# Kernel tuning notes

Measured on AMD Instinct MI355X. Metric: run time of the kernel, lower is better.

The kernel has to match this reference:

```python
import jax, jax.numpy as jnp
import numpy as np

N, E, F_IN, H, C = 10000, 640000, 128, 128, 40


def setup_inputs() -> dict:
    key = jax.random.key(0)
    ks = jax.random.split(key, 8)
    x = jax.random.normal(ks[0], (N, F_IN), dtype=jnp.float32)
    edge_index = jax.random.randint(ks[1], (2, E), 0, N, dtype=jnp.int64)
    W1 = jax.random.normal(ks[2], (F_IN, H), dtype=jnp.float32) / np.sqrt(F_IN)
    b1 = jnp.zeros((H,), dtype=jnp.float32)
    W2 = jax.random.normal(ks[3], (H, H), dtype=jnp.float32) / np.sqrt(H)
    b2 = jnp.zeros((H,), dtype=jnp.float32)
    Wc = jax.random.normal(ks[4], (H, C), dtype=jnp.float32) / np.sqrt(H)
    bc = jnp.zeros((C,), dtype=jnp.float32)
    return {"x": x, "edge_index": edge_index, "W1": W1, "b1": b1,
            "W2": W2, "b2": b2, "Wc": Wc, "bc": bc}


def _gcn_conv(x, src, dst, norm, W, b):
    # GCNConv: out = D^{-1/2}(A+I)D^{-1/2} (x @ W) + b
    h = x @ W                               # [N, H]
    msg = h[src] * norm[:, None]            # gather + per-edge normalize
    out = jax.ops.segment_sum(msg, dst, num_segments=N)  # scatter-add
    return out + b


def reference(x, edge_index, W1, b1, W2, b2, Wc, bc):
    # add self-loops (as PyG GCNConv does by default)
    loops = jnp.arange(N, dtype=edge_index.dtype)
    src = jnp.concatenate([edge_index[0], loops])   # [E+N]
    dst = jnp.concatenate([edge_index[1], loops])   # [E+N]
    # symmetric normalization deg^{-1/2} with self-loops included
    deg = jax.ops.segment_sum(jnp.ones_like(dst, dtype=x.dtype), dst, num_segments=N)
    dinv = jax.lax.rsqrt(deg)                       # deg >= 1 due to self-loops
    norm = dinv[src] * dinv[dst]                    # [E+N]

    h = _gcn_conv(x, src, dst, norm, W1, b1)
    h = jax.nn.relu(h)
    h = _gcn_conv(h, src, dst, norm, W2, b2)
    logits = h @ Wc + bc                            # [N, C]
    return jax.nn.log_softmax(logits, axis=1)
```

## Files before the change

kernel.cpp:

```cpp
#include <hip/hip_runtime.h>
#include <hip/hip_fp16.h>
#include <math.h>

#define FDIM 128
#define CDIM 40
#define DMAX 192
#define NMAX 10240
#define SLICE_SHIFT 14
#define SLICE_SZ (1 << SLICE_SHIFT)

__device__ __forceinline__ uint2 pack_half4(float4 v) {
    __half2 p0 = __float22half2_rn(make_float2(v.x, v.y));
    __half2 p1 = __float22half2_rn(make_float2(v.z, v.w));
    uint2 u;
    u.x = *(unsigned int*)&p0;
    u.y = *(unsigned int*)&p1;
    return u;
}

__device__ __forceinline__ void upadd(float& a0, float& a1, unsigned int u) {
    __half2 h = *(__half2*)&u;
    float2 f = __half22float2(h);
    a0 += f.x; a1 += f.y;
}

__global__ __launch_bounds__(1024) void k_hist(
        const int* __restrict__ dst, unsigned short* __restrict__ lrank,
        int* __restrict__ cnt, int e, int n) {
    __shared__ int h[NMAX];
    int tid = threadIdx.x;
    for (int i = tid; i < n; i += 1024) h[i] = 0;
    __syncthreads();
    int base = (int)blockIdx.x << SLICE_SHIFT;
    int end = base + SLICE_SZ; if (end > e) end = e;
    for (int i = base + tid * 4; i < end; i += 4096) {
        if (i + 3 < end) {
            int4 d = *(const int4*)(dst + i);
            int p0 = atomicAdd(&h[d.x], 1);
            int p1 = atomicAdd(&h[d.y], 1);
            int p2 = atomicAdd(&h[d.z], 1);
            int p3 = atomicAdd(&h[d.w], 1);
            ushort4 r;
            r.x = (unsigned short)p0; r.y = (unsigned short)p1;
            r.z = (unsigned short)p2; r.w = (unsigned short)p3;
            *(ushort4*)(lrank + i) = r;
        } else {
            for (int k = i; k < end; ++k)
                lrank[k] = (unsigned short)atomicAdd(&h[dst[k]], 1);
        }
    }
    __syncthreads();
    int* c = cnt + (size_t)blockIdx.x * n;
    for (int i = tid; i < n; i += 1024) c[i] = h[i];
}

__global__ __launch_bounds__(256) void k_scan(
        int* __restrict__ cnt, int* __restrict__ deg, int nslice, int n) {
    int v = blockIdx.x * 256 + threadIdx.x;
    if (v >= n) return;
    int s = 0;
    for (int b = 0; b < nslice; ++b) {
        int t = cnt[(size_t)b * n + v];
        cnt[(size_t)b * n + v] = s;
        s += t;
    }
    deg[v] = s;
}

__global__ __launch_bounds__(256) void k_mega(
        const float* __restrict__ A, const float* __restrict__ W,
        const int* __restrict__ deg, uint2* __restrict__ h16, int n,
        const int* __restrict__ src, const int* __restrict__ dst,
        const unsigned short* __restrict__ lrank, const int* __restrict__ base,
        unsigned short* __restrict__ col, int e, int gemm_blocks) {
    __shared__ float As[32][FDIM];
    int tid = threadIdx.x;
    if ((int)blockIdx.x < gemm_blocks) {
        int r0 = blockIdx.x * 32;
        for (int t = tid; t < 32 * 32; t += 256) {
            int r = t >> 5, c4 = t & 31;
            int gr = r0 + r;
            float4 v = make_float4(0.f, 0.f, 0.f, 0.f);
            if (gr < n) v = ((const float4*)A)[(size_t)gr * 32 + c4];
            ((float4*)As[r])[c4] = v;
        }
        __syncthreads();
        int cb = (tid & 31) * 4;
        int rb = (tid >> 5) * 4;
        float4 acc0 = make_float4(0,0,0,0), acc1 = acc0, acc2 = acc0, acc3 = acc0;
        for (int k = 0; k < FDIM; ++k) {
            float4 w = *(const float4*)(W + k * FDIM + cb);
            float a0 = As[rb + 0][k], a1 = As[rb + 1][k];
            float a2 = As[rb + 2][k], a3 = As[rb + 3][k];
            acc0.x += a0 * w.x; acc0.y += a0 * w.y; acc0.z += a0 * w.z; acc0.w += a0 * w.w;
            acc1.x += a1 * w.x; acc1.y += a1 * w.y; acc1.z += a1 * w.z; acc1.w += a1 * w.w;
            acc2.x += a2 * w.x; acc2.y += a2 * w.y; acc2.z += a2 * w.z; acc2.w += a2 * w.w;
            acc3.x += a3 * w.x; acc3.y += a3 * w.y; acc3.z += a3 * w.z; acc3.w += a3 * w.w;
        }
        float4 accs[4] = {acc0, acc1, acc2, acc3};
        #pragma unroll
        for (int i = 0; i < 4; ++i) {
            int gr = r0 + rb + i;
            if (gr < n) {
                float dinv = rsqrtf((float)(deg[gr] + 1));
                float4 v = accs[i];
                v.x *= dinv; v.y *= dinv; v.z *= dinv; v.w *= dinv;
                h16[(size_t)gr * 32 + (cb >> 2)] = pack_half4(v);
            }
        }
    } else {
        int g = ((int)blockIdx.x - gemm_blocks) * 256 + tid;
        int i4 = g * 4;
        if (i4 + 3 < e) {
            const int* bs = base + (size_t)(i4 >> SLICE_SHIFT) * n;
            int4 d = ((const int4*)dst)[g];
            int4 s = ((const int4*)src)[g];
            ushort4 lr = ((const ushort4*)lrank)[g];
            int p0 = bs[d.x] + lr.x;
            int p1 = bs[d.y] + lr.y;
            int p2 = bs[d.z] + lr.z;
            int p3 = bs[d.w] + lr.w;
            if (p0 < DMAX) col[(size_t)d.x * DMAX + p0] = (unsigned short)s.x;
            if (p1 < DMAX) col[(size_t)d.y * DMAX + p1] = (unsigned short)s.y;
            if (p2 < DMAX) col[(size_t)d.z * DMAX + p2] = (unsigned short)s.z;
            if (p3 < DMAX) col[(size_t)d.w * DMAX + p3] = (unsigned short)s.w;
        } else if (i4 < e) {
            for (int k = i4; k < e; ++k) {
                int d = dst[k];
                int p = base[(size_t)(k >> SLICE_SHIFT) * n + d] + lrank[k];
                if (p < DMAX) col[(size_t)d * DMAX + p] = (unsigned short)src[k];
            }
        }
    }
}

__device__ __forceinline__ void wave_gather(
        float& o0, float& o1, const unsigned int* __restrict__ hs,
        const unsigned short* __restrict__ col, int node, int dn, int lane) {
    float a0 = 0.f, a1 = 0.f, b0 = 0.f, b1 = 0.f;
    upadd(a0, a1, hs[(size_t)node * 64 + lane]);
    const uint4* cl8 = (const uint4*)(col + (size_t)node * DMAX);
    int j = 0;
    for (; j + 16 <= dn; j += 16) {
        uint4 cA = cl8[(j >> 3)];
        uint4 cB = cl8[(j >> 3) + 1];
        int s0 = cA.x & 0xFFFF, s1 = cA.x >> 16;
        int s2 = cA.y & 0xFFFF, s3 = cA.y >> 16;
        int s4 = cA.z & 0xFFFF, s5 = cA.z >> 16;
        int s6 = cA.w & 0xFFFF, s7 = cA.w >> 16;
        int s8 = cB.x & 0xFFFF, s9 = cB.x >> 16;
        int sa = cB.y & 0xFFFF, sb = cB.y >> 16;
        int sc = cB.z & 0xFFFF, sd = cB.z >> 16;
        int se = cB.w & 0xFFFF, sf = cB.w >> 16;
        unsigned int q0 = hs[(size_t)s0 * 64 + lane];
        unsigned int q1 = hs[(size_t)s1 * 64 + lane];
        unsigned int q2 = hs[(size_t)s2 * 64 + lane];
        unsigned int q3 = hs[(size_t)s3 * 64 + lane];
        unsigned int q4 = hs[(size_t)s4 * 64 + lane];
        unsigned int q5 = hs[(size_t)s5 * 64 + lane];
        unsigned int q6 = hs[(size_t)s6 * 64 + lane];
        unsigned int q7 = hs[(size_t)s7 * 64 + lane];
        unsigned int q8 = hs[(size_t)s8 * 64 + lane];
        unsigned int q9 = hs[(size_t)s9 * 64 + lane];
        unsigned int qa = hs[(size_t)sa * 64 + lane];
        unsigned int qb = hs[(size_t)sb * 64 + lane];
        unsigned int qc = hs[(size_t)sc * 64 + lane];
        unsigned int qd = hs[(size_t)sd * 64 + lane];
        unsigned int qe = hs[(size_t)se * 64 + lane];
        unsigned int qf = hs[(size_t)sf * 64 + lane];
        upadd(a0, a1, q0); upadd(b0, b1, q1);
        upadd(a0, a1, q2); upadd(b0, b1, q3);
        upadd(a0, a1, q4); upadd(b0, b1, q5);
        upadd(a0, a1, q6); upadd(b0, b1, q7);
        upadd(a0, a1, q8); upadd(b0, b1, q9);
        upadd(a0, a1, qa); upadd(b0, b1, qb);
        upadd(a0, a1, qc); upadd(b0, b1, qd);
        upadd(a0, a1, qe); upadd(b0, b1, qf);
    }
    for (; j + 8 <= dn; j += 8) {
        uint4 c = cl8[j >> 3];
        int s0 = c.x & 0xFFFF, s1 = c.x >> 16;
        int s2 = c.y & 0xFFFF, s3 = c.y >> 16;
        int s4 = c.z & 0xFFFF, s5 = c.z >> 16;
        int s6 = c.w & 0xFFFF, s7 = c.w >> 16;
        unsigned int q0 = hs[(size_t)s0 * 64 + lane];
        unsigned int q1 = hs[(size_t)s1 * 64 + lane];
        unsigned int q2 = hs[(size_t)s2 * 64 + lane];
        unsigned int q3 = hs[(size_t)s3 * 64 + lane];
        unsigned int q4 = hs[(size_t)s4 * 64 + lane];
        unsigned int q5 = hs[(size_t)s5 * 64 + lane];
        unsigned int q6 = hs[(size_t)s6 * 64 + lane];
        unsigned int q7 = hs[(size_t)s7 * 64 + lane];
        upadd(a0, a1, q0); upadd(b0, b1, q1);
        upadd(a0, a1, q2); upadd(b0, b1, q3);
        upadd(a0, a1, q4); upadd(b0, b1, q5);
        upadd(a0, a1, q6); upadd(b0, b1, q7);
    }
    const unsigned short* cl = col + (size_t)node * DMAX;
    for (; j < dn; ++j) upadd(a0, a1, hs[(size_t)cl[j] * 64 + lane]);
    o0 = a0 + b0;
    o1 = a1 + b1;
}

__global__ __launch_bounds__(512) void k_agg1(
        const unsigned int* __restrict__ hs1, const unsigned short* __restrict__ col,
        const int* __restrict__ deg, const float* __restrict__ b1,
        float* __restrict__ a1, int n) {
    int node = (blockIdx.x * 512 + threadIdx.x) >> 6;
    int lane = threadIdx.x & 63;
    if (node >= n) return;
    int dn = deg[node];
    float dinv = rsqrtf((float)(dn + 1));
    if (dn > DMAX) dn = DMAX;
    float o0, o1;
    wave_gather(o0, o1, hs1, col, node, dn, lane);
    float2 bb = ((const float2*)b1)[lane];
    float v0 = fmaxf(dinv * o0 + bb.x, 0.f);
    float v1 = fmaxf(dinv * o1 + bb.y, 0.f);
    ((float2*)a1)[(size_t)node * 64 + lane] = make_float2(v0, v1);
}

__global__ __launch_bounds__(256) void k_gemm2(
        const float* __restrict__ A, const float* __restrict__ W,
        const int* __restrict__ deg, uint2* __restrict__ h16, int n) {
    __shared__ float As[32][FDIM];
    int tid = threadIdx.x;
    int r0 = blockIdx.x * 32;
    for (int t = tid; t < 32 * 32; t += 256) {
        int r = t >> 5, c4 = t & 31;
        int gr = r0 + r;
        float4 v = make_float4(0.f, 0.f, 0.f, 0.f);
        if (gr < n) v = ((const float4*)A)[(size_t)gr * 32 + c4];
        ((float4*)As[r])[c4] = v;
    }
    __syncthreads();
    int cb = (tid & 31) * 4;
    int rb = (tid >> 5) * 4;
    float4 acc0 = make_float4(0,0,0,0), acc1 = acc0, acc2 = acc0, acc3 = acc0;
    for (int k = 0; k < FDIM; ++k) {
        float4 w = *(const float4*)(W + k * FDIM + cb);
        float a0 = As[rb + 0][k], a1 = As[rb + 1][k];
        float a2 = As[rb + 2][k], a3 = As[rb + 3][k];
        acc0.x += a0 * w.x; acc0.y += a0 * w.y; acc0.z += a0 * w.z; acc0.w += a0 * w.w;
        acc1.x += a1 * w.x; acc1.y += a1 * w.y; acc1.z += a1 * w.z; acc1.w += a1 * w.w;
        acc2.x += a2 * w.x; acc2.y += a2 * w.y; acc2.z += a2 * w.z; acc2.w += a2 * w.w;
        acc3.x += a3 * w.x; acc3.y += a3 * w.y; acc3.z += a3 * w.z; acc3.w += a3 * w.w;
    }
    float4 accs[4] = {acc0, acc1, acc2, acc3};
    #pragma unroll
    for (int i = 0; i < 4; ++i) {
        int gr = r0 + rb + i;
        if (gr < n) {
            float dinv = rsqrtf((float)(deg[gr] + 1));
            float4 v = accs[i];
            v.x *= dinv; v.y *= dinv; v.z *= dinv; v.w *= dinv;
            h16[(size_t)gr * 32 + (cb >> 2)] = pack_half4(v);
        }
    }
}

__global__ __launch_bounds__(512) void k_agg2c(
        const unsigned int* __restrict__ hs2, const unsigned short* __restrict__ col,
        const int* __restrict__ deg, const float* __restrict__ b2,
        const float* __restrict__ Wc, const float* __restrict__ bc,
        float* __restrict__ out, int n) {
    __shared__ float As[8][FDIM];
    int tid = threadIdx.x;
    int wv = tid >> 6, lane = tid & 63;
    int node = blockIdx.x * 8 + wv;
    if (node < n) {
        int dn = deg[node];
        float dinv = rsqrtf((float)(dn + 1));
        if (dn > DMAX) dn = DMAX;
        float o0, o1;
        wave_gather(o0, o1, hs2, col, node, dn, lane);
        float2 bb = ((const float2*)b2)[lane];
        ((float2*)As[wv])[lane] = make_float2(dinv * o0 + bb.x, dinv * o1 + bb.y);
    }
    __syncthreads();
    if (node >= n) return;
    const float* row = As[wv];
    int c = (lane < CDIM) ? lane : (lane - 24);
    float acc = bc[c];
    for (int k = 0; k < FDIM; k += 4) {
        float a0 = row[k + 0], a1 = row[k + 1];
        float a2 = row[k + 2], a3 = row[k + 3];
        acc += a0 * Wc[(k + 0) * CDIM + c];
        acc += a1 * Wc[(k + 1) * CDIM + c];
        acc += a2 * Wc[(k + 2) * CDIM + c];
        acc += a3 * Wc[(k + 3) * CDIM + c];
    }
    float lv = (lane < CDIM) ? acc : -INFINITY;
    float m = lv;
    for (int off = 32; off > 0; off >>= 1) m = fmaxf(m, __shfl_down(m, off));
    m = __shfl(m, 0);
    float e = (lane < CDIM) ? expf(lv - m) : 0.0f;
    float s = e;
    for (int off = 32; off > 0; off >>= 1) s += __shfl_down(s, off);
    s = __shfl(s, 0);
    if (lane < CDIM) out[(size_t)node * CDIM + lane] = lv - m - logf(s);
}


extern "C" void kernel_launch(void* const* d_in, const int* in_sizes, int n_in,
                              void* d_out, int out_size, void* d_ws, size_t ws_size,
                              hipStream_t stream) {
    const float* x  = (const float*)d_in[0];
    const int*   ei = (const int*)d_in[1];
    const float* W1 = (const float*)d_in[2];
    const float* b1 = (const float*)d_in[3];
    const float* W2 = (const float*)d_in[4];
    const float* b2 = (const float*)d_in[5];
    const float* Wc = (const float*)d_in[6];
    const float* bc = (const float*)d_in[7];
    float* out = (float*)d_out;

    const int N = in_sizes[0] / FDIM;
    const int E = in_sizes[1] / 2;
    const int* srcp = ei;
    const int* dstp = ei + E;
    const int NSLICE = (E + SLICE_SZ - 1) >> SLICE_SHIFT;

    char* ws = (char*)d_ws;
    auto alloc = [&](size_t bytes) {
        char* p = ws;
        ws += (bytes + 255) & ~(size_t)255;
        return p;
    };
    int*            deg   = (int*)           alloc((size_t)N * 4);
    int*            cnt   = (int*)           alloc((size_t)NSLICE * N * 4);
    unsigned short* lrank = (unsigned short*)alloc((size_t)E * 2);
    unsigned short* col   = (unsigned short*)alloc((size_t)N * DMAX * 2);
    uint4*          h1h   = (uint4*)         alloc((size_t)N * 256);
    uint4*          h2h   = (uint4*)         alloc((size_t)N * 256);
    float*          a1    = (float*)         alloc((size_t)N * FDIM * 4);

    k_hist<<<NSLICE, 1024, 0, stream>>>(dstp, lrank, cnt, E, N);

    k_scan<<<(N + 255) / 256, 256, 0, stream>>>(cnt, deg, NSLICE, N);

    int gb = (N + 31) / 32;
    int fb = (E / 4 + 255) / 256;
    k_mega<<<gb + fb, 256, 0, stream>>>(
        x, W1, deg, (uint2*)h1h, N, srcp, dstp, lrank, cnt, col, E, gb);

    k_agg1<<<((size_t)N * 64 + 511) / 512, 512, 0, stream>>>(
        (const unsigned int*)h1h, col, deg, b1, a1, N);

    k_gemm2<<<(N + 31) / 32, 256, 0, stream>>>(
        a1, W2, deg, (uint2*)h2h, N);

    k_agg2c<<<(N + 7) / 8, 512, 0, stream>>>(
        (const unsigned int*)h2h, col, deg, b2, Wc, bc, out, N);
}
```

Baseline: 157.9 us.

## Replace fixed-width padded adjacency with compact CSR using atomic row offsets

The per-node adjacency storage moves from a fixed DMAX=192 padded slab to a compact CSR. Each node's row start comes from an atomicAdd on a global counter in the scan kernel, with rows padded to multiples of 8. This drops the degree cap, so correctness no longer depends on the degree bound, and it shrinks the column array footprint. It also uses a nontemporal store for the layer-1 activations and removes a __syncthreads in the final aggregation kernel, which relies on each wave reading only its own shared-memory row. The cost is an extra start[] lookup per edge, and row placement now depends on atomic ordering, which can scatter rows.

```diff
diff --git a/kernel.cpp b/kernel.cpp
--- a/kernel.cpp
+++ b/kernel.cpp
@@ -4,10 +4,11 @@
 
 #define FDIM 128
 #define CDIM 40
-#define DMAX 192
 #define NMAX 10240
 #define SLICE_SHIFT 14
 #define SLICE_SZ (1 << SLICE_SHIFT)
+
+typedef float evf2 __attribute__((ext_vector_type(2)));
 
 __device__ __forceinline__ uint2 pack_half4(float4 v) {
     __half2 p0 = __float22half2_rn(make_float2(v.x, v.y));
@@ -26,9 +27,10 @@
 
 __global__ __launch_bounds__(1024) void k_hist(
         const int* __restrict__ dst, unsigned short* __restrict__ lrank,
-        int* __restrict__ cnt, int e, int n) {
+        int* __restrict__ cnt, int* __restrict__ ctr, int e, int n) {
     __shared__ int h[NMAX];
     int tid = threadIdx.x;
+    if (blockIdx.x == 0 && tid == 0) *ctr = 0;
     for (int i = tid; i < n; i += 1024) h[i] = 0;
     __syncthreads();
     int base = (int)blockIdx.x << SLICE_SHIFT;
@@ -55,7 +57,8 @@
 }
 
 __global__ __launch_bounds__(256) void k_scan(
-        int* __restrict__ cnt, int* __restrict__ deg, int nslice, int n) {
+        int* __restrict__ cnt, int* __restrict__ deg, int* __restrict__ start,
+        int* __restrict__ ctr, int nslice, int n) {
     int v = blockIdx.x * 256 + threadIdx.x;
     if (v >= n) return;
     int s = 0;
@@ -65,6 +68,8 @@
         s += t;
     }
     deg[v] = s;
+    int p8 = (s + 7) & ~7;
+    start[v] = atomicAdd(ctr, p8);
 }
 
 __global__ __launch_bounds__(256) void k_mega(
@@ -72,7 +77,8 @@
         const int* __restrict__ deg, uint2* __restrict__ h16, int n,
         const int* __restrict__ src, const int* __restrict__ dst,
         const unsigned short* __restrict__ lrank, const int* __restrict__ base,
-        unsigned short* __restrict__ col, int e, int gemm_blocks) {
+        const int* __restrict__ start, unsigned short* __restrict__ col,
+        int e, int gemm_blocks) {
     __shared__ float As[32][FDIM];
     int tid = threadIdx.x;
     if ((int)blockIdx.x < gemm_blocks) {
@@ -116,19 +122,19 @@
             int4 d = ((const int4*)dst)[g];
             int4 s = ((const int4*)src)[g];
             ushort4 lr = ((const ushort4*)lrank)[g];
-            int p0 = bs[d.x] + lr.x;
-            int p1 = bs[d.y] + lr.y;
-            int p2 = bs[d.z] + lr.z;
-            int p3 = bs[d.w] + lr.w;
-            if (p0 < DMAX) col[(size_t)d.x * DMAX + p0] = (unsigned short)s.x;
-            if (p1 < DMAX) col[(size_t)d.y * DMAX + p1] = (unsigned short)s.y;
-            if (p2 < DMAX) col[(size_t)d.z * DMAX + p2] = (unsigned short)s.z;
-            if (p3 < DMAX) col[(size_t)d.w * DMAX + p3] = (unsigned short)s.w;
+            int p0 = start[d.x] + bs[d.x] + lr.x;
+            int p1 = start[d.y] + bs[d.y] + lr.y;
+            int p2 = start[d.z] + bs[d.z] + lr.z;
+            int p3 = start[d.w] + bs[d.w] + lr.w;
+            col[p0] = (unsigned short)s.x;
+            col[p1] = (unsigned short)s.y;
+            col[p2] = (unsigned short)s.z;
+            col[p3] = (unsigned short)s.w;
         } else if (i4 < e) {
             for (int k = i4; k < e; ++k) {
                 int d = dst[k];
-                int p = base[(size_t)(k >> SLICE_SHIFT) * n + d] + lrank[k];
-                if (p < DMAX) col[(size_t)d * DMAX + p] = (unsigned short)src[k];
+                int p = start[d] + base[(size_t)(k >> SLICE_SHIFT) * n + d] + lrank[k];
+                col[p] = (unsigned short)src[k];
             }
         }
     }
@@ -136,10 +142,10 @@
 
 __device__ __forceinline__ void wave_gather(
         float& o0, float& o1, const unsigned int* __restrict__ hs,
-        const unsigned short* __restrict__ col, int node, int dn, int lane) {
+        const unsigned short* __restrict__ row, int node, int dn, int lane) {
     float a0 = 0.f, a1 = 0.f, b0 = 0.f, b1 = 0.f;
     upadd(a0, a1, hs[(size_t)node * 64 + lane]);
-    const uint4* cl8 = (const uint4*)(col + (size_t)node * DMAX);
+    const uint4* cl8 = (const uint4*)row;
     int j = 0;
     for (; j + 16 <= dn; j += 16) {
         uint4 cA = cl8[(j >> 3)];
@@ -196,28 +202,27 @@
         upadd(a0, a1, q4); upadd(b0, b1, q5);
         upadd(a0, a1, q6); upadd(b0, b1, q7);
     }
-    const unsigned short* cl = col + (size_t)node * DMAX;
-    for (; j < dn; ++j) upadd(a0, a1, hs[(size_t)cl[j] * 64 + lane]);
+    for (; j < dn; ++j) upadd(a0, a1, hs[(size_t)row[j] * 64 + lane]);
     o0 = a0 + b0;
     o1 = a1 + b1;
 }
 
 __global__ __launch_bounds__(512) void k_agg1(
-        const unsigned int* __restrict__ hs1, const unsigned short* __restrict__ col,
-        const int* __restrict__ deg, const float* __restrict__ b1,
-        float* __restrict__ a1, int n) {
+        const unsigned int* __restrict__ hs1, const unsigned short* __restrict__ csr,
+        const int* __restrict__ deg, const int* __restrict__ start,
+        const float* __restrict__ b1, float* __restrict__ a1, int n) {
     int node = (blockIdx.x * 512 + threadIdx.x) >> 6;
     int lane = threadIdx.x & 63;
     if (node >= n) return;
     int dn = deg[node];
     float dinv = rsqrtf((float)(dn + 1));
-    if (dn > DMAX) dn = DMAX;
     float o0, o1;
-    wave_gather(o0, o1, hs1, col, node, dn, lane);
+    wave_gather(o0, o1, hs1, csr + start[node], node, dn, lane);
     float2 bb = ((const float2*)b1)[lane];
-    float v0 = fmaxf(dinv * o0 + bb.x, 0.f);
-    float v1 = fmaxf(dinv * o1 + bb.y, 0.f);
-    ((float2*)a1)[(size_t)node * 64 + lane] = make_float2(v0, v1);
+    evf2 v;
+    v.x = fmaxf(dinv * o0 + bb.x, 0.f);
+    v.y = fmaxf(dinv * o1 + bb.y, 0.f);
+    __builtin_nontemporal_store(v, &((evf2*)a1)[(size_t)node * 64 + lane]);
 }
 
 __global__ __launch_bounds__(256) void k_gemm2(
@@ -260,25 +265,23 @@
 }
 
 __global__ __launch_bounds__(512) void k_agg2c(
-        const unsigned int* __restrict__ hs2, const unsigned short* __restrict__ col,
-        const int* __restrict__ deg, const float* __restrict__ b2,
-        const float* __restrict__ Wc, const float* __restrict__ bc,
-        float* __restrict__ out, int n) {
+        const unsigned int* __restrict__ hs2, const unsigned short* __restrict__ csr,
+        const int* __restrict__ deg, const int* __restrict__ start,
+        const float* __restrict__ b2, const float* __restrict__ Wc,
+        const float* __restrict__ bc, float* __restrict__ out, int n) {
     __shared__ float As[8][FDIM];
     int tid = threadIdx.x;
     int wv = tid >> 6, lane = tid & 63;
     int node = blockIdx.x * 8 + wv;
-    if (node < n) {
+    if (node >= n) return;
+    {
         int dn = deg[node];
         float dinv = rsqrtf((float)(dn + 1));
-        if (dn > DMAX) dn = DMAX;
         float o0, o1;
-        wave_gather(o0, o1, hs2, col, node, dn, lane);
+        wave_gather(o0, o1, hs2, csr + start[node], node, dn, lane);
         float2 bb = ((const float2*)b2)[lane];
         ((float2*)As[wv])[lane] = make_float2(dinv * o0 + bb.x, dinv * o1 + bb.y);
     }
-    __syncthreads();
-    if (node >= n) return;
     const float* row = As[wv];
     int c = (lane < CDIM) ? lane : (lane - 24);
     float acc = bc[c];
@@ -328,28 +331,30 @@
         return p;
     };
     int*            deg   = (int*)           alloc((size_t)N * 4);
+    int*            start = (int*)           alloc((size_t)N * 4);
+    int*            ctr   = (int*)           alloc(256);
     int*            cnt   = (int*)           alloc((size_t)NSLICE * N * 4);
     unsigned short* lrank = (unsigned short*)alloc((size_t)E * 2);
-    unsigned short* col   = (unsigned short*)alloc((size_t)N * DMAX * 2);
+    unsigned short* col   = (unsigned short*)alloc((size_t)E * 2 + (size_t)N * 16);
     uint4*          h1h   = (uint4*)         alloc((size_t)N * 256);
     uint4*          h2h   = (uint4*)         alloc((size_t)N * 256);
     float*          a1    = (float*)         alloc((size_t)N * FDIM * 4);
 
-    k_hist<<<NSLICE, 1024, 0, stream>>>(dstp, lrank, cnt, E, N);
-
-    k_scan<<<(N + 255) / 256, 256, 0, stream>>>(cnt, deg, NSLICE, N);
+    k_hist<<<NSLICE, 1024, 0, stream>>>(dstp, lrank, cnt, ctr, E, N);
+
+    k_scan<<<(N + 255) / 256, 256, 0, stream>>>(cnt, deg, start, ctr, NSLICE, N);
 
     int gb = (N + 31) / 32;
     int fb = (E / 4 + 255) / 256;
     k_mega<<<gb + fb, 256, 0, stream>>>(
-        x, W1, deg, (uint2*)h1h, N, srcp, dstp, lrank, cnt, col, E, gb);
+        x, W1, deg, (uint2*)h1h, N, srcp, dstp, lrank, cnt, start, col, E, gb);
 
     k_agg1<<<((size_t)N * 64 + 511) / 512, 512, 0, stream>>>(
-        (const unsigned int*)h1h, col, deg, b1, a1, N);
+        (const unsigned int*)h1h, col, deg, start, b1, a1, N);
 
     k_gemm2<<<(N + 31) / 32, 256, 0, stream>>>(
         a1, W2, deg, (uint2*)h2h, N);
 
     k_agg2c<<<(N + 7) / 8, 512, 0, stream>>>(
-        (const unsigned int*)h2h, col, deg, b2, Wc, bc, out, N);
-}
+        (const unsigned int*)h2h, col, deg, start, b2, Wc, bc, out, N);
+}
```

New measurement: 163.9 us. 1.04x slower.

## Fold classifier weights into second GCN layer to aggregate 40-wide features

Applied to the files above, without the earlier changes.

Since layer 2 has no nonlinearity before the classifier, W2·Wc and b2·Wc+bc are precomputed (inside the scan kernel's extra blocks) so the second GEMM produces 40-wide fp32 features instead of 128-wide fp16. The second aggregation then gathers 40 floats per neighbor and applies bias and log_softmax directly, with no per-node classifier GEMM. This cuts gather bytes and compute in the heaviest stage, but changes the rounding order and switches the gathered values to fp32, and lanes 40..63 read beyond each row, which relies on the padding added to the z allocation.

```diff
diff --git a/kernel.cpp b/kernel.cpp
--- a/kernel.cpp
+++ b/kernel.cpp
@@ -54,17 +54,37 @@
     for (int i = tid; i < n; i += 1024) c[i] = h[i];
 }
 
-__global__ __launch_bounds__(256) void k_scan(
-        int* __restrict__ cnt, int* __restrict__ deg, int nslice, int n) {
-    int v = blockIdx.x * 256 + threadIdx.x;
-    if (v >= n) return;
-    int s = 0;
-    for (int b = 0; b < nslice; ++b) {
-        int t = cnt[(size_t)b * n + v];
-        cnt[(size_t)b * n + v] = s;
-        s += t;
-    }
-    deg[v] = s;
+__global__ __launch_bounds__(256) void k_scan_wc(
+        int* __restrict__ cnt, int* __restrict__ deg, int nslice, int n,
+        int scanB, const float* __restrict__ W2, const float* __restrict__ Wc,
+        const float* __restrict__ b2, const float* __restrict__ bc,
+        float* __restrict__ W2c, float* __restrict__ bias2c) {
+    int tid = threadIdx.x;
+    if ((int)blockIdx.x < scanB) {
+        int v = blockIdx.x * 256 + tid;
+        if (v >= n) return;
+        int s = 0;
+        for (int b = 0; b < nslice; ++b) {
+            int t = cnt[(size_t)b * n + v];
+            cnt[(size_t)b * n + v] = s;
+            s += t;
+        }
+        deg[v] = s;
+    } else {
+        int o = ((int)blockIdx.x - scanB) * 256 + tid;
+        if (o >= FDIM * CDIM) return;
+        int k = o / CDIM, c = o - k * CDIM;
+        float acc = 0.f;
+        for (int j = 0; j < FDIM; ++j)
+            acc += W2[k * FDIM + j] * Wc[j * CDIM + c];
+        W2c[o] = acc;
+        if (o < CDIM) {
+            float b = bc[o];
+            for (int j = 0; j < FDIM; ++j)
+                b += b2[j] * Wc[j * CDIM + o];
+            bias2c[o] = b;
+        }
+    }
 }
 
 __global__ __launch_bounds__(256) void k_mega(
@@ -220,77 +240,111 @@
     ((float2*)a1)[(size_t)node * 64 + lane] = make_float2(v0, v1);
 }
 
-__global__ __launch_bounds__(256) void k_gemm2(
-        const float* __restrict__ A, const float* __restrict__ W,
-        const int* __restrict__ deg, uint2* __restrict__ h16, int n) {
+__global__ __launch_bounds__(320) void k_gemm2c(
+        const float* __restrict__ A, const float* __restrict__ W2c,
+        const int* __restrict__ deg, float* __restrict__ z, int n) {
     __shared__ float As[32][FDIM];
+    __shared__ float Ws[FDIM * CDIM];
     int tid = threadIdx.x;
     int r0 = blockIdx.x * 32;
-    for (int t = tid; t < 32 * 32; t += 256) {
+    for (int t = tid; t < 32 * 32; t += 320) {
         int r = t >> 5, c4 = t & 31;
         int gr = r0 + r;
         float4 v = make_float4(0.f, 0.f, 0.f, 0.f);
         if (gr < n) v = ((const float4*)A)[(size_t)gr * 32 + c4];
         ((float4*)As[r])[c4] = v;
     }
+    for (int t = tid; t < FDIM * CDIM; t += 320) Ws[t] = W2c[t];
     __syncthreads();
-    int cb = (tid & 31) * 4;
-    int rb = (tid >> 5) * 4;
-    float4 acc0 = make_float4(0,0,0,0), acc1 = acc0, acc2 = acc0, acc3 = acc0;
+    int c = tid % CDIM;
+    int g = tid / CDIM;
+    int rb = g * 4;
+    float acc0 = 0.f, acc1 = 0.f, acc2 = 0.f, acc3 = 0.f;
     for (int k = 0; k < FDIM; ++k) {
-        float4 w = *(const float4*)(W + k * FDIM + cb);
-        float a0 = As[rb + 0][k], a1 = As[rb + 1][k];
-        float a2 = As[rb + 2][k], a3 = As[rb + 3][k];
-        acc0.x += a0 * w.x; acc0.y += a0 * w.y; acc0.z += a0 * w.z; acc0.w += a0 * w.w;
-        acc1.x += a1 * w.x; acc1.y += a1 * w.y; acc1.z += a1 * w.z; acc1.w += a1 * w.w;
-        acc2.x += a2 * w.x; acc2.y += a2 * w.y; acc2.z += a2 * w.z; acc2.w += a2 * w.w;
-        acc3.x += a3 * w.x; acc3.y += a3 * w.y; acc3.z += a3 * w.z; acc3.w += a3 * w.w;
-    }
-    float4 accs[4] = {acc0, acc1, acc2, acc3};
+        float w = Ws[k * CDIM + c];
+        acc0 += As[rb + 0][k] * w;
+        acc1 += As[rb + 1][k] * w;
+        acc2 += As[rb + 2][k] * w;
+        acc3 += As[rb + 3][k] * w;
+    }
+    float accs[4] = {acc0, acc1, acc2, acc3};
     #pragma unroll
     for (int i = 0; i < 4; ++i) {
         int gr = r0 + rb + i;
         if (gr < n) {
             float dinv = rsqrtf((float)(deg[gr] + 1));
-            float4 v = accs[i];
-            v.x *= dinv; v.y *= dinv; v.z *= dinv; v.w *= dinv;
-            h16[(size_t)gr * 32 + (cb >> 2)] = pack_half4(v);
-        }
-    }
-}
-
-__global__ __launch_bounds__(512) void k_agg2c(
-        const unsigned int* __restrict__ hs2, const unsigned short* __restrict__ col,
-        const int* __restrict__ deg, const float* __restrict__ b2,
-        const float* __restrict__ Wc, const float* __restrict__ bc,
+            z[(size_t)gr * CDIM + c] = dinv * accs[i];
+        }
+    }
+}
+
+__global__ __launch_bounds__(512) void k_agg2s(
+        const float* __restrict__ z, const unsigned short* __restrict__ col,
+        const int* __restrict__ deg, const float* __restrict__ bias2c,
         float* __restrict__ out, int n) {
-    __shared__ float As[8][FDIM];
     int tid = threadIdx.x;
     int wv = tid >> 6, lane = tid & 63;
     int node = blockIdx.x * 8 + wv;
-    if (node < n) {
-        int dn = deg[node];
-        float dinv = rsqrtf((float)(dn + 1));
-        if (dn > DMAX) dn = DMAX;
-        float o0, o1;
-        wave_gather(o0, o1, hs2, col, node, dn, lane);
-        float2 bb = ((const float2*)b2)[lane];
-        ((float2*)As[wv])[lane] = make_float2(dinv * o0 + bb.x, dinv * o1 + bb.y);
-    }
-    __syncthreads();
     if (node >= n) return;
-    const float* row = As[wv];
-    int c = (lane < CDIM) ? lane : (lane - 24);
-    float acc = bc[c];
-    for (int k = 0; k < FDIM; k += 4) {
-        float a0 = row[k + 0], a1 = row[k + 1];
-        float a2 = row[k + 2], a3 = row[k + 3];
-        acc += a0 * Wc[(k + 0) * CDIM + c];
-        acc += a1 * Wc[(k + 1) * CDIM + c];
-        acc += a2 * Wc[(k + 2) * CDIM + c];
-        acc += a3 * Wc[(k + 3) * CDIM + c];
-    }
-    float lv = (lane < CDIM) ? acc : -INFINITY;
+    int dn = deg[node];
+    float dinv = rsqrtf((float)(dn + 1));
+    if (dn > DMAX) dn = DMAX;
+    const uint4* cl8 = (const uint4*)(col + (size_t)node * DMAX);
+    float a = z[(size_t)node * CDIM + lane];
+    float b = 0.f;
+    int j = 0;
+    for (; j + 16 <= dn; j += 16) {
+        uint4 cA = cl8[(j >> 3)];
+        uint4 cB = cl8[(j >> 3) + 1];
+        int s0 = cA.x & 0xFFFF, s1 = cA.x >> 16;
+        int s2 = cA.y & 0xFFFF, s3 = cA.y >> 16;
+        int s4 = cA.z & 0xFFFF, s5 = cA.z >> 16;
+        int s6 = cA.w & 0xFFFF, s7 = cA.w >> 16;
+        int s8 = cB.x & 0xFFFF, s9 = cB.x >> 16;
+        int sa = cB.y & 0xFFFF, sb = cB.y >> 16;
+        int sc = cB.z & 0xFFFF, sd = cB.z >> 16;
+        int se = cB.w & 0xFFFF, sf = cB.w >> 16;
+        float q0 = z[(size_t)s0 * CDIM + lane];
+        float q1 = z[(size_t)s1 * CDIM + lane];
+        float q2 = z[(size_t)s2 * CDIM + lane];
+        float q3 = z[(size_t)s3 * CDIM + lane];
+        float q4 = z[(size_t)s4 * CDIM + lane];
+        float q5 = z[(size_t)s5 * CDIM + lane];
+        float q6 = z[(size_t)s6 * CDIM + lane];
+        float q7 = z[(size_t)s7 * CDIM + lane];
+        float q8 = z[(size_t)s8 * CDIM + lane];
+        float q9 = z[(size_t)s9 * CDIM + lane];
+        float qa = z[(size_t)sa * CDIM + lane];
+        float qb = z[(size_t)sb * CDIM + lane];
+        float qc = z[(size_t)sc * CDIM + lane];
+        float qd = z[(size_t)sd * CDIM + lane];
+        float qe = z[(size_t)se * CDIM + lane];
+        float qf = z[(size_t)sf * CDIM + lane];
+        a += q0; b += q1; a += q2; b += q3;
+        a += q4; b += q5; a += q6; b += q7;
+        a += q8; b += q9; a += qa; b += qb;
+        a += qc; b += qd; a += qe; b += qf;
+    }
+    for (; j + 8 <= dn; j += 8) {
+        uint4 c = cl8[j >> 3];
+        int s0 = c.x & 0xFFFF, s1 = c.x >> 16;
+        int s2 = c.y & 0xFFFF, s3 = c.y >> 16;
+        int s4 = c.z & 0xFFFF, s5 = c.z >> 16;
+        int s6 = c.w & 0xFFFF, s7 = c.w >> 16;
+        float q0 = z[(size_t)s0 * CDIM + lane];
+        float q1 = z[(size_t)s1 * CDIM + lane];
+        float q2 = z[(size_t)s2 * CDIM + lane];
+        float q3 = z[(size_t)s3 * CDIM + lane];
+        float q4 = z[(size_t)s4 * CDIM + lane];
+        float q5 = z[(size_t)s5 * CDIM + lane];
+        float q6 = z[(size_t)s6 * CDIM + lane];
+        float q7 = z[(size_t)s7 * CDIM + lane];
+        a += q0; b += q1; a += q2; b += q3;
+        a += q4; b += q5; a += q6; b += q7;
+    }
+    const unsigned short* cl = col + (size_t)node * DMAX;
+    for (; j < dn; ++j) a += z[(size_t)cl[j] * CDIM + lane];
+    float lv = (lane < CDIM) ? (dinv * (a + b) + bias2c[lane]) : -INFINITY;
     float m = lv;
     for (int off = 32; off > 0; off >>= 1) m = fmaxf(m, __shfl_down(m, off));
     m = __shfl(m, 0);
@@ -327,17 +381,22 @@
         ws += (bytes + 255) & ~(size_t)255;
         return p;
     };
-    int*            deg   = (int*)           alloc((size_t)N * 4);
-    int*            cnt   = (int*)           alloc((size_t)NSLICE * N * 4);
-    unsigned short* lrank = (unsigned short*)alloc((size_t)E * 2);
-    unsigned short* col   = (unsigned short*)alloc((size_t)N * DMAX * 2);
-    uint4*          h1h   = (uint4*)         alloc((size_t)N * 256);
-    uint4*          h2h   = (uint4*)         alloc((size_t)N * 256);
-    float*          a1    = (float*)         alloc((size_t)N * FDIM * 4);
+    int*            deg    = (int*)           alloc((size_t)N * 4);
+    int*            cnt    = (int*)           alloc((size_t)NSLICE * N * 4);
+    unsigned short* lrank  = (unsigned short*)alloc((size_t)E * 2);
+    unsigned short* col    = (unsigned short*)alloc((size_t)N * DMAX * 2);
+    uint4*          h1h    = (uint4*)         alloc((size_t)N * 256);
+    float*          a1     = (float*)         alloc((size_t)N * FDIM * 4);
+    float*          W2c    = (float*)         alloc((size_t)FDIM * CDIM * 4);
+    float*          bias2c = (float*)         alloc((size_t)CDIM * 4);
+    float*          z      = (float*)         alloc((size_t)N * CDIM * 4 + 256);
 
     k_hist<<<NSLICE, 1024, 0, stream>>>(dstp, lrank, cnt, E, N);
 
-    k_scan<<<(N + 255) / 256, 256, 0, stream>>>(cnt, deg, NSLICE, N);
+    int scanB = (N + 255) / 256;
+    int wcB = (FDIM * CDIM + 255) / 256;
+    k_scan_wc<<<scanB + wcB, 256, 0, stream>>>(
+        cnt, deg, NSLICE, N, scanB, W2, Wc, b2, bc, W2c, bias2c);
 
     int gb = (N + 31) / 32;
     int fb = (E / 4 + 255) / 256;
@@ -347,9 +406,7 @@
     k_agg1<<<((size_t)N * 64 + 511) / 512, 512, 0, stream>>>(
         (const unsigned int*)h1h, col, deg, b1, a1, N);
 
-    k_gemm2<<<(N + 31) / 32, 256, 0, stream>>>(
-        a1, W2, deg, (uint2*)h2h, N);
-
-    k_agg2c<<<(N + 7) / 8, 512, 0, stream>>>(
-        (const unsigned int*)h2h, col, deg, b2, Wc, bc, out, N);
-}
+    k_gemm2c<<<(N + 31) / 32, 320, 0, stream>>>(a1, W2c, deg, z, N);
+
+    k_agg2s<<<(N + 7) / 8, 512, 0, stream>>>(z, col, deg, bias2c, out, N);
+}
```

Measured after the change: 148.2 us. -6.1%, faster.
